# Performance work log

Hardware: AMD Instinct MI355X
Metric: run time of the kernel (lower is better)

The kernel has to match this reference:

```python
import jax, jax.numpy as jnp
import numpy as np

DIM = 512
HEADS = 8
HEAD_DIM = DIM // HEADS
SCALE = HEAD_DIM ** -0.5


def setup_inputs() -> dict:
    key = jax.random.key(0)
    ks = jax.random.split(key, 7)
    B, QN, N = 32, 128, 4096
    q = jax.random.normal(ks[0], (B, QN, DIM), dtype=jnp.float32)
    kv = jax.random.normal(ks[1], (B, N, DIM), dtype=jnp.float32)
    key_mask = jax.random.normal(ks[2], (B, QN, N), dtype=jnp.float32)
    Wq = jax.random.normal(ks[3], (DIM, DIM), dtype=jnp.float32) * 0.02
    Wkv = jax.random.normal(ks[4], (2 * DIM, DIM), dtype=jnp.float32) * 0.02
    Wproj = jax.random.normal(ks[5], (DIM, DIM), dtype=jnp.float32) * 0.02
    bproj = jax.random.normal(ks[6], (DIM,), dtype=jnp.float32) * 0.02
    return {"q": q, "kv": kv, "key_mask": key_mask,
            "Wq": Wq, "Wkv": Wkv, "Wproj": Wproj, "bproj": bproj}


def reference(q, kv, key_mask, Wq, Wkv, Wproj, bproj):
    B, QN, C = q.shape
    N = kv.shape[1]
    # q projection -> [B, QN, H, hd]
    qh = (q @ Wq.T).reshape(B, QN, HEADS, HEAD_DIM) * SCALE
    # kv projection -> split into k, v each [B, N, H, hd]
    kvp = kv @ Wkv.T  # [B, N, 2C]
    k = kvp[..., :C].reshape(B, N, HEADS, HEAD_DIM)
    v = kvp[..., C:].reshape(B, N, HEADS, HEAD_DIM)
    # scores [B, H, QN, N] + additive mask broadcast over heads
    attn = jnp.einsum('bqhd,bkhd->bhqk', qh, k) + key_mask[:, None]
    attn = jax.nn.softmax(attn, axis=-1)
    x = jnp.einsum('bhqk,bkhd->bqhd', attn, v).reshape(B, QN, C)
    return x @ Wproj.T + bproj
```

## Files before the change

### kernel.cpp

```cpp
#include <hip/hip_runtime.h>
#include <hip/hip_bf16.h>

typedef __attribute__((ext_vector_type(4))) float f32x4;
typedef __attribute__((ext_vector_type(8))) short bf16x8;

#define GAS __attribute__((address_space(1)))
#define LAS __attribute__((address_space(3)))

__device__ __forceinline__ unsigned int cvtpk(float lo, float hi) {
  unsigned int r;
  asm("v_cvt_pk_bf16_f32 %0, %1, %2" : "=v"(r) : "v"(lo), "v"(hi));
  return r;
}
__device__ __forceinline__ unsigned short f2bf(float f) { return (unsigned short)cvtpk(f, f); }
__device__ __forceinline__ f32x4 mfma16(bf16x8 a, bf16x8 b, f32x4 c) {
  return __builtin_amdgcn_mfma_f32_16x16x32_bf16(a, b, c, 0, 0, 0);
}
__device__ __forceinline__ void gl_lds16(const unsigned short* g, unsigned short* l) {
  __builtin_amdgcn_global_load_lds((const GAS unsigned short*)g, (LAS unsigned short*)l, 16, 0, 0);
}
__device__ __forceinline__ void memfence_sched() { asm volatile("" ::: "memory"); }

__global__ __launch_bounds__(256)
void cvt_f32_bf16(const float* __restrict__ in, unsigned short* __restrict__ out, int n8) {
  for (int i = blockIdx.x * blockDim.x + threadIdx.x; i < n8; i += gridDim.x * blockDim.x) {
    const float4 a = *reinterpret_cast<const float4*>(in + (size_t)i * 8);
    const float4 b = *reinterpret_cast<const float4*>(in + (size_t)i * 8 + 4);
    uint4 o;
    o.x = cvtpk(a.x, a.y); o.y = cvtpk(a.z, a.w);
    o.z = cvtpk(b.x, b.y); o.w = cvtpk(b.z, b.w);
    *reinterpret_cast<uint4*>(out + (size_t)i * 8) = o;
  }
}

template<int MODE, bool AF32, bool BF32>
__global__ __launch_bounds__(512, 2)
void gemm8(const void* __restrict__ Agv, const void* __restrict__ Bgv,
           void* __restrict__ Cg, const float* __restrict__ bias, int ntn, size_t ldc)
{
  constexpr bool MIXED = AF32 || BF32;
  constexpr int NA = MIXED ? 2 : 3;
  constexpr int NB = MIXED ? 2 : 3;
  __shared__ unsigned short sm[(NA + NB) * 8192];
  unsigned short* const smB = sm + NA * 8192;

  const int t = threadIdx.x, lane = t & 63, w = t >> 6;
  const int lo = lane & 15, hi = lane >> 4;
  const int wm = w >> 2, wn = w & 3;
  const int nwg = gridDim.x, bid = blockIdx.x;
  const int id = (bid & 7) * (nwg >> 3) + (bid >> 3);
  const int row0 = (id / ntn) * 256, col0 = (id % ntn) * 256;
  const int w16 = w * 16;

  const unsigned short* Ab = (const unsigned short*)Agv;
  const unsigned short* Bb = (const unsigned short*)Bgv;
  const float* Ff = AF32 ? (const float*)Agv : (const float*)Bgv;
  const int frow0 = AF32 ? row0 : col0;

  const int cxor_g = (lane >> 3) & 3;
  const size_t a_src_g = (size_t)(row0 + w16 + (lane >> 2)) * 512 + (((lane & 3) ^ cxor_g) << 3);
  const size_t b_src_g = (size_t)(col0 + w16 + (lane >> 2)) * 512 + (((lane & 3) ^ cxor_g) << 3);

  const int rs_r = t >> 2;
  const int rs_c = (t & 3) * 8;
  const int wch = ((t & 3) ^ ((t >> 3) & 3)) << 3;

  float4 stF[2][4];

  auto F_ISSUE = [&](int kt) {
    if constexpr (MIXED) {
      const int bk = kt & 1;
      const float* s0 = Ff + (size_t)(frow0 + rs_r) * 512 + kt * 32 + rs_c;
      const float* s1 = Ff + (size_t)(frow0 + 128 + rs_r) * 512 + kt * 32 + rs_c;
      stF[bk][0] = *(const float4*)s0; stF[bk][1] = *(const float4*)(s0 + 4);
      stF[bk][2] = *(const float4*)s1; stF[bk][3] = *(const float4*)(s1 + 4);
    }
  };
  auto F_WRITE = [&](int kt) {
    if constexpr (MIXED) {
      const int bk = kt & 1;
      unsigned short* fb = AF32 ? &sm[(kt % NA) * 8192] : &smB[(kt % NB) * 8192];
      uint4 o;
      o.x = cvtpk(stF[bk][0].x, stF[bk][0].y); o.y = cvtpk(stF[bk][0].z, stF[bk][0].w);
      o.z = cvtpk(stF[bk][1].x, stF[bk][1].y); o.w = cvtpk(stF[bk][1].z, stF[bk][1].w);
      *reinterpret_cast<uint4*>(&fb[rs_r * 32 + wch]) = o;
      o.x = cvtpk(stF[bk][2].x, stF[bk][2].y); o.y = cvtpk(stF[bk][2].z, stF[bk][2].w);
      o.z = cvtpk(stF[bk][3].x, stF[bk][3].y); o.w = cvtpk(stF[bk][3].z, stF[bk][3].w);
      *reinterpret_cast<uint4*>(&fb[(128 + rs_r) * 32 + wch]) = o;
    }
  };
  auto G_ISSUE = [&](int kt) {
    if constexpr (!AF32) {
      unsigned short* ab = &sm[(kt % NA) * 8192];
      gl_lds16(Ab + a_src_g + kt * 32, ab + w16 * 32);
      gl_lds16(Ab + a_src_g + (size_t)128 * 512 + kt * 32, ab + (128 + w16) * 32);
    }
    if constexpr (!BF32) {
      unsigned short* bb = &smB[(kt % NB) * 8192];
      gl_lds16(Bb + b_src_g + kt * 32, bb + w16 * 32);
      gl_lds16(Bb + b_src_g + (size_t)128 * 512 + kt * 32, bb + (128 + w16) * 32);
    }
  };

  f32x4 acc[8][4] = {};
  const int fxor = (hi ^ ((lo >> 1) & 3)) << 3;

  if constexpr (MIXED) {
    F_ISSUE(0);
    G_ISSUE(0);
    F_ISSUE(1);
    memfence_sched();
    asm volatile("s_waitcnt vmcnt(6)" ::: "memory");
    F_WRITE(0);
    asm volatile("s_waitcnt vmcnt(4)" ::: "memory");
  } else {
    G_ISSUE(0); G_ISSUE(1);
    memfence_sched();
    asm volatile("s_waitcnt vmcnt(4)" ::: "memory");
  }
  asm volatile("s_waitcnt lgkmcnt(0)" ::: "memory");
  __builtin_amdgcn_s_barrier();
  memfence_sched();

  #pragma unroll
  for (int kt = 0; kt < 16; ++kt) {
    const unsigned short* ab = &sm[(kt % NA) * 8192];
    const unsigned short* bb = &smB[(kt % NB) * 8192];
    bf16x8 bfr[4], af[4];
    #pragma unroll
    for (int nj = 0; nj < 4; ++nj)
      bfr[nj] = *reinterpret_cast<const bf16x8*>(&bb[(wn * 64 + nj * 16 + lo) * 32 + fxor]);
    #pragma unroll
    for (int mi = 0; mi < 4; ++mi)
      af[mi] = *reinterpret_cast<const bf16x8*>(&ab[(wm * 128 + mi * 16 + lo) * 32 + fxor]);

    if constexpr (MIXED) {
      if (kt <= 14) G_ISSUE(kt + 1);
      if (kt <= 13) F_ISSUE(kt + 2);
    } else {
      if (kt <= 13) G_ISSUE(kt + 2);
    }
    memfence_sched();

    __builtin_amdgcn_s_setprio(1);
    #pragma unroll
    for (int mi = 0; mi < 4; ++mi)
      #pragma unroll
      for (int nj = 0; nj < 4; ++nj)
        acc[mi][nj] = mfma16(af[mi], bfr[nj], acc[mi][nj]);
    __builtin_amdgcn_s_setprio(0);

    #pragma unroll
    for (int mi = 0; mi < 4; ++mi)
      af[mi] = *reinterpret_cast<const bf16x8*>(&ab[(wm * 128 + (mi + 4) * 16 + lo) * 32 + fxor]);

    if constexpr (MIXED) {
      if (kt <= 13)      { asm volatile("s_waitcnt vmcnt(6)" ::: "memory"); }
      else if (kt == 14) { asm volatile("s_waitcnt vmcnt(2)" ::: "memory"); }
      if (kt <= 14) F_WRITE(kt + 1);
    }

    __builtin_amdgcn_s_setprio(1);
    #pragma unroll
    for (int mi = 0; mi < 4; ++mi)
      #pragma unroll
      for (int nj = 0; nj < 4; ++nj)
        acc[mi + 4][nj] = mfma16(af[mi], bfr[nj], acc[mi + 4][nj]);
    __builtin_amdgcn_s_setprio(0);

    if (kt < 15) {
      if constexpr (MIXED) {
        if (kt <= 13)      { asm volatile("s_waitcnt vmcnt(4)" ::: "memory"); }
        else               { asm volatile("s_waitcnt vmcnt(0)" ::: "memory"); }
      } else {
        if (kt <= 13)      { asm volatile("s_waitcnt vmcnt(4)" ::: "memory"); }
        else               { asm volatile("s_waitcnt vmcnt(0)" ::: "memory"); }
      }
      asm volatile("s_waitcnt lgkmcnt(0)" ::: "memory");
      __builtin_amdgcn_s_barrier();
      memfence_sched();
    }
  }

  #pragma unroll
  for (int mi = 0; mi < 8; ++mi) {
    #pragma unroll
    for (int r = 0; r < 4; ++r) {
      const size_t gm = (size_t)row0 + wm * 128 + mi * 16 + hi * 4 + r;
      #pragma unroll
      for (int nj = 0; nj < 4; ++nj) {
        const int gn = col0 + wn * 64 + nj * 16 + lo;
        const float v = acc[mi][nj][r];
        if constexpr (MODE == 0)
          ((unsigned short*)Cg)[gm * ldc + gn] = f2bf(v * 0.125f);
        else if constexpr (MODE == 1)
          ((unsigned short*)Cg)[gm * ldc + gn] = f2bf(v);
        else
          ((float*)Cg)[gm * ldc + gn] = v + bias[gn];
      }
    }
  }
}

__global__ __launch_bounds__(256)
void attn_fwd(const unsigned short* __restrict__ qh,
              const unsigned short* __restrict__ kbuf,
              const unsigned short* __restrict__ vT,
              const float* __restrict__ mask,
              float* __restrict__ opart, float* __restrict__ ml)
{
  __shared__ unsigned short Ks[64 * 64];
  __shared__ unsigned short Vs[64 * 64];
  __shared__ unsigned short Ps[4][16 * 64];
  const int bid = blockIdx.x;
  const int xcd = bid & 7, g = bid >> 3;
  const int b = (g >> 6) * 8 + xcd;
  const int sub = g & 63;
  const int h = sub >> 3, qhalf = (sub >> 2) & 1, c = sub & 3;
  const int n0 = c * 1024;
  const int bh2 = (b * 8 + h) * 2 + qhalf;
  const int t = threadIdx.x, lane = t & 63, w = t >> 6;
  const int hi = lane >> 4, lo = lane & 15;
  const int q0 = qhalf * 64 + w * 16;

  bf16x8 aq[2];
  #pragma unroll
  for (int kk = 0; kk < 2; ++kk)
    aq[kk] = *reinterpret_cast<const bf16x8*>(
        qh + (size_t)(b * 128 + q0 + lo) * 512 + h * 64 + kk * 32 + hi * 8);

  float mrow[4], lrow[4];
  #pragma unroll
  for (int i = 0; i < 4; ++i) { mrow[i] = -1e30f; lrow[i] = 0.f; }
  f32x4 o[4] = {};

  const unsigned short* kp = kbuf + ((size_t)b * 4096 + n0) * 512 + h * 64;
  const unsigned short* vp = vT + (size_t)(h * 64) * 131072 + (size_t)b * 4096 + n0;
  const float* mp = mask + ((size_t)(b * 128 + q0)) * 4096 + n0;

  for (int nt = 0; nt < 16; ++nt) {
    {
      const int r = t >> 3, cc = t & 7;
      *reinterpret_cast<uint4*>(&Ks[r * 64 + ((cc ^ (r & 7)) << 3)]) =
          *reinterpret_cast<const uint4*>(kp + (size_t)(nt * 64 + r) * 512 + (cc << 3));
      *reinterpret_cast<uint4*>(&Ks[(r + 32) * 64 + ((cc ^ (r & 7)) << 3)]) =
          *reinterpret_cast<const uint4*>(kp + (size_t)(nt * 64 + r + 32) * 512 + (cc << 3));
      *reinterpret_cast<uint4*>(&Vs[r * 64 + ((cc ^ (r & 7)) << 3)]) =
          *reinterpret_cast<const uint4*>(vp + (size_t)r * 131072 + nt * 64 + (cc << 3));
      *reinterpret_cast<uint4*>(&Vs[(r + 32) * 64 + ((cc ^ (r & 7)) << 3)]) =
          *reinterpret_cast<const uint4*>(vp + (size_t)(r + 32) * 131072 + nt * 64 + (cc << 3));
    }
    __syncthreads();

    f32x4 s[4] = {};
    __builtin_amdgcn_s_setprio(1);
    #pragma unroll
    for (int ni = 0; ni < 4; ++ni) {
      #pragma unroll
      for (int kk = 0; kk < 2; ++kk) {
        const bf16x8 kf = *reinterpret_cast<const bf16x8*>(
            &Ks[(ni * 16 + lo) * 64 + ((kk * 32 + hi * 8) ^ ((lo & 7) << 3))]);
        s[ni] = mfma16(aq[kk], kf, s[ni]);
      }
    }
    __builtin_amdgcn_s_setprio(0);
    #pragma unroll
    for (int ni = 0; ni < 4; ++ni)
      #pragma unroll
      for (int r = 0; r < 4; ++r)
        s[ni][r] += mp[(size_t)(hi * 4 + r) * 4096 + nt * 64 + ni * 16 + lo];

    #pragma unroll
    for (int r = 0; r < 4; ++r) {
      float mx = fmaxf(fmaxf(s[0][r], s[1][r]), fmaxf(s[2][r], s[3][r]));
      #pragma unroll
      for (int off = 1; off < 16; off <<= 1)
        mx = fmaxf(mx, __shfl_xor(mx, off, 64));
      const float mnew = fmaxf(mrow[r], mx);
      const float corr = __expf(mrow[r] - mnew);
      mrow[r] = mnew;
      float ls = 0.f;
      #pragma unroll
      for (int ni = 0; ni < 4; ++ni) {
        const float p = __expf(s[ni][r] - mnew);
        s[ni][r] = p; ls += p;
      }
      #pragma unroll
      for (int off = 1; off < 16; off <<= 1)
        ls += __shfl_xor(ls, off, 64);
      lrow[r] = lrow[r] * corr + ls;
      #pragma unroll
      for (int di = 0; di < 4; ++di)
        o[di][r] *= corr;
    }

    #pragma unroll
    for (int ni = 0; ni < 4; ++ni)
      #pragma unroll
      for (int r = 0; r < 4; ++r) {
        const int rp = hi * 4 + r;
        Ps[w][rp * 64 + ((ni * 16 + lo) ^ ((rp & 7) << 3))] = f2bf(s[ni][r]);
      }

    __builtin_amdgcn_s_setprio(1);
    #pragma unroll
    for (int kk = 0; kk < 2; ++kk) {
      const bf16x8 pa = *reinterpret_cast<const bf16x8*>(
          &Ps[w][lo * 64 + ((kk * 32 + hi * 8) ^ ((lo & 7) << 3))]);
      #pragma unroll
      for (int di = 0; di < 4; ++di) {
        const bf16x8 vf = *reinterpret_cast<const bf16x8*>(
            &Vs[(di * 16 + lo) * 64 + ((kk * 32 + hi * 8) ^ ((lo & 7) << 3))]);
        o[di] = mfma16(pa, vf, o[di]);
      }
    }
    __builtin_amdgcn_s_setprio(0);
    __syncthreads();
  }

  const size_t pbase = ((size_t)bh2 * 4 + c) * 64;
  #pragma unroll
  for (int di = 0; di < 4; ++di)
    #pragma unroll
    for (int r = 0; r < 4; ++r)
      opart[(pbase + (w * 16 + hi * 4 + r)) * 64 + di * 16 + lo] = o[di][r];
  if (lo == 0) {
    #pragma unroll
    for (int r = 0; r < 4; ++r) {
      const int qq = w * 16 + hi * 4 + r;
      ml[(((size_t)bh2 * 4 + c) * 2 + 0) * 64 + qq] = mrow[r];
      ml[(((size_t)bh2 * 4 + c) * 2 + 1) * 64 + qq] = lrow[r];
    }
  }
}

__global__ __launch_bounds__(256)
void attn_combine(const float* __restrict__ opart, const float* __restrict__ ml,
                  unsigned short* __restrict__ xb)
{
  const int bh2 = blockIdx.x;
  const int b = bh2 >> 4, h = (bh2 >> 1) & 7, qhalf = bh2 & 1;
  const int t = threadIdx.x;
  const int q = t >> 2, dg = t & 3;

  float m[4], l[4];
  #pragma unroll
  for (int c = 0; c < 4; ++c) {
    m[c] = ml[(((size_t)bh2 * 4 + c) * 2 + 0) * 64 + q];
    l[c] = ml[(((size_t)bh2 * 4 + c) * 2 + 1) * 64 + q];
  }
  const float M = fmaxf(fmaxf(m[0], m[1]), fmaxf(m[2], m[3]));
  float sc[4], L = 0.f;
  #pragma unroll
  for (int c = 0; c < 4; ++c) { sc[c] = __expf(m[c] - M); L += sc[c] * l[c]; }
  const float inv = 1.f / L;

  float4 acc[4] = {};
  #pragma unroll
  for (int c = 0; c < 4; ++c) {
    const float* base = opart + (((size_t)bh2 * 4 + c) * 64 + q) * 64 + dg * 16;
    #pragma unroll
    for (int j = 0; j < 4; ++j) {
      const float4 v = *reinterpret_cast<const float4*>(base + j * 4);
      acc[j].x = fmaf(sc[c], v.x, acc[j].x);
      acc[j].y = fmaf(sc[c], v.y, acc[j].y);
      acc[j].z = fmaf(sc[c], v.z, acc[j].z);
      acc[j].w = fmaf(sc[c], v.w, acc[j].w);
    }
  }
  unsigned short* dst = xb + ((size_t)b * 128 + qhalf * 64 + q) * 512 + h * 64 + dg * 16;
  uint4 o1, o2;
  o1.x = cvtpk(acc[0].x * inv, acc[0].y * inv); o1.y = cvtpk(acc[0].z * inv, acc[0].w * inv);
  o1.z = cvtpk(acc[1].x * inv, acc[1].y * inv); o1.w = cvtpk(acc[1].z * inv, acc[1].w * inv);
  o2.x = cvtpk(acc[2].x * inv, acc[2].y * inv); o2.y = cvtpk(acc[2].z * inv, acc[2].w * inv);
  o2.z = cvtpk(acc[3].x * inv, acc[3].y * inv); o2.w = cvtpk(acc[3].z * inv, acc[3].w * inv);
  *reinterpret_cast<uint4*>(dst) = o1;
  *reinterpret_cast<uint4*>(dst + 8) = o2;
}

extern "C" void kernel_launch(void* const* d_in, const int* in_sizes, int n_in,
                              void* d_out, int out_size, void* d_ws, size_t ws_size,
                              hipStream_t stream) {
  const float* q     = (const float*)d_in[0];
  const float* kv    = (const float*)d_in[1];
  const float* mask  = (const float*)d_in[2];
  const float* Wq    = (const float*)d_in[3];
  const float* Wkv   = (const float*)d_in[4];
  const float* Wproj = (const float*)d_in[5];
  const float* bproj = (const float*)d_in[6];
  float* out = (float*)d_out;

  char* ws = (char*)d_ws;
  unsigned short* kbuf   = (unsigned short*)ws;
  unsigned short* vTb    = (unsigned short*)(ws + 134217728ULL);
  float*          opart  = (float*)(ws + 268435456ULL);
  float*          mlb    = (float*)(ws + 301989888ULL);
  unsigned short* qhb    = (unsigned short*)(ws + 303038464ULL);
  unsigned short* xb     = (unsigned short*)(ws + 307232768ULL);
  unsigned short* Wqb    = (unsigned short*)(ws + 311427072ULL);
  unsigned short* Wkvb   = (unsigned short*)(ws + 311951360ULL);
  unsigned short* Wprojb = (unsigned short*)(ws + 312999936ULL);

  cvt_f32_bf16<<<128, 256, 0, stream>>>(Wq, Wqb, 512 * 512 / 8);
  cvt_f32_bf16<<<256, 256, 0, stream>>>(Wkv, Wkvb, 1024 * 512 / 8);
  cvt_f32_bf16<<<128, 256, 0, stream>>>(Wproj, Wprojb, 512 * 512 / 8);

  gemm8<0, true, false><<<32, 512, 0, stream>>>(q, Wqb, qhb, nullptr, 2, 512);
  gemm8<1, true, false><<<1024, 512, 0, stream>>>(kv, Wkvb, kbuf, nullptr, 2, 512);
  gemm8<1, false, true><<<1024, 512, 0, stream>>>(Wkvb + 512 * 512, kv, vTb, nullptr, 512, 131072);
  attn_fwd<<<2048, 256, 0, stream>>>(qhb, kbuf, vTb, mask, opart, mlb);
  attn_combine<<<512, 256, 0, stream>>>(opart, mlb, xb);
  gemm8<2, false, false><<<32, 512, 0, stream>>>(xb, Wprojb, out, bproj, 2, 512);
}
```

Baseline: 448.9 us.

## Pre-convert activations to bf16 and use a pure-bf16 async-staged GEMM

Removes the fp32-input register staging path from the GEMM. q and kv are now converted to bf16 in separate passes, with kv done in two chunks that reuse the opart workspace. The GEMM now stages A and B separately through global_load_lds with a new LDS layout and a three-deep buffer ring, interleaving barriers between the half-tile MFMA phases. The extra conversion passes add an fp32 read and a bf16 write of kv. The GEMM loads become fully asynchronous, at the cost of more barriers per k-step.

```diff
diff --git a/kernel.cpp b/kernel.cpp
--- a/kernel.cpp
+++ b/kernel.cpp
@@ -33,115 +33,63 @@
   }
 }
 
-template<int MODE, bool AF32, bool BF32>
+template<int MODE>
 __global__ __launch_bounds__(512, 2)
-void gemm8(const void* __restrict__ Agv, const void* __restrict__ Bgv,
-           void* __restrict__ Cg, const float* __restrict__ bias, int ntn, size_t ldc)
+void gemm8p(const unsigned short* __restrict__ Ag, const unsigned short* __restrict__ Bg,
+            void* __restrict__ Cg, const float* __restrict__ bias, int ntn, size_t ldc)
 {
-  constexpr bool MIXED = AF32 || BF32;
-  constexpr int NA = MIXED ? 2 : 3;
-  constexpr int NB = MIXED ? 2 : 3;
-  __shared__ unsigned short sm[(NA + NB) * 8192];
-  unsigned short* const smB = sm + NA * 8192;
-
+  __shared__ unsigned short sm[49152];
   const int t = threadIdx.x, lane = t & 63, w = t >> 6;
   const int lo = lane & 15, hi = lane >> 4;
   const int wm = w >> 2, wn = w & 3;
   const int nwg = gridDim.x, bid = blockIdx.x;
   const int id = (bid & 7) * (nwg >> 3) + (bid >> 3);
   const int row0 = (id / ntn) * 256, col0 = (id % ntn) * 256;
-  const int w16 = w * 16;
-
-  const unsigned short* Ab = (const unsigned short*)Agv;
-  const unsigned short* Bb = (const unsigned short*)Bgv;
-  const float* Ff = AF32 ? (const float*)Agv : (const float*)Bgv;
-  const int frow0 = AF32 ? row0 : col0;
-
-  const int cxor_g = (lane >> 3) & 3;
-  const size_t a_src_g = (size_t)(row0 + w16 + (lane >> 2)) * 512 + (((lane & 3) ^ cxor_g) << 3);
-  const size_t b_src_g = (size_t)(col0 + w16 + (lane >> 2)) * 512 + (((lane & 3) ^ cxor_g) << 3);
-
-  const int rs_r = t >> 2;
-  const int rs_c = (t & 3) * 8;
-  const int wch = ((t & 3) ^ ((t >> 3) & 3)) << 3;
-
-  float4 stF[2][4];
-
-  auto F_ISSUE = [&](int kt) {
-    if constexpr (MIXED) {
-      const int bk = kt & 1;
-      const float* s0 = Ff + (size_t)(frow0 + rs_r) * 512 + kt * 32 + rs_c;
-      const float* s1 = Ff + (size_t)(frow0 + 128 + rs_r) * 512 + kt * 32 + rs_c;
-      stF[bk][0] = *(const float4*)s0; stF[bk][1] = *(const float4*)(s0 + 4);
-      stF[bk][2] = *(const float4*)s1; stF[bk][3] = *(const float4*)(s1 + 4);
-    }
+
+  const int gcol = ((t & 3) * 8) ^ (((t >> 5) & 1) << 4);
+  const int grow = t >> 2;
+  const unsigned short* aS = Ag + (size_t)(row0 + grow) * 512 + gcol;
+  const unsigned short* bS = Bg + (size_t)(col0 + grow) * 512 + gcol;
+  const int wds = w * 512;
+
+  auto STAGE_A = [&](int kt) {
+    const int bf = kt % 3;
+    gl_lds16(aS + kt * 32,         &sm[(bf * 2 + 0) * 4096 + wds]);
+    gl_lds16(aS + kt * 32 + 65536, &sm[(bf * 2 + 1) * 4096 + wds]);
   };
-  auto F_WRITE = [&](int kt) {
-    if constexpr (MIXED) {
-      const int bk = kt & 1;
-      unsigned short* fb = AF32 ? &sm[(kt % NA) * 8192] : &smB[(kt % NB) * 8192];
-      uint4 o;
-      o.x = cvtpk(stF[bk][0].x, stF[bk][0].y); o.y = cvtpk(stF[bk][0].z, stF[bk][0].w);
-      o.z = cvtpk(stF[bk][1].x, stF[bk][1].y); o.w = cvtpk(stF[bk][1].z, stF[bk][1].w);
-      *reinterpret_cast<uint4*>(&fb[rs_r * 32 + wch]) = o;
-      o.x = cvtpk(stF[bk][2].x, stF[bk][2].y); o.y = cvtpk(stF[bk][2].z, stF[bk][2].w);
-      o.z = cvtpk(stF[bk][3].x, stF[bk][3].y); o.w = cvtpk(stF[bk][3].z, stF[bk][3].w);
-      *reinterpret_cast<uint4*>(&fb[(128 + rs_r) * 32 + wch]) = o;
-    }
+  auto STAGE_B = [&](int kt) {
+    const int bf = kt % 3;
+    gl_lds16(bS + kt * 32,         &sm[24576 + (bf * 2 + 0) * 4096 + wds]);
+    gl_lds16(bS + kt * 32 + 65536, &sm[24576 + (bf * 2 + 1) * 4096 + wds]);
   };
-  auto G_ISSUE = [&](int kt) {
-    if constexpr (!AF32) {
-      unsigned short* ab = &sm[(kt % NA) * 8192];
-      gl_lds16(Ab + a_src_g + kt * 32, ab + w16 * 32);
-      gl_lds16(Ab + a_src_g + (size_t)128 * 512 + kt * 32, ab + (128 + w16) * 32);
-    }
-    if constexpr (!BF32) {
-      unsigned short* bb = &smB[(kt % NB) * 8192];
-      gl_lds16(Bb + b_src_g + kt * 32, bb + w16 * 32);
-      gl_lds16(Bb + b_src_g + (size_t)128 * 512 + kt * 32, bb + (128 + w16) * 32);
-    }
-  };
 
   f32x4 acc[8][4] = {};
-  const int fxor = (hi ^ ((lo >> 1) & 3)) << 3;
-
-  if constexpr (MIXED) {
-    F_ISSUE(0);
-    G_ISSUE(0);
-    F_ISSUE(1);
-    memfence_sched();
-    asm volatile("s_waitcnt vmcnt(6)" ::: "memory");
-    F_WRITE(0);
-    asm volatile("s_waitcnt vmcnt(4)" ::: "memory");
-  } else {
-    G_ISSUE(0); G_ISSUE(1);
-    memfence_sched();
-    asm volatile("s_waitcnt vmcnt(4)" ::: "memory");
-  }
-  asm volatile("s_waitcnt lgkmcnt(0)" ::: "memory");
+  const int fc = (hi * 8) ^ (((lo >> 3) & 1) << 4);
+  const int rbB = (wn & 1) * 64;
+
+  STAGE_A(0); STAGE_B(0); STAGE_A(1); STAGE_B(1);
+  memfence_sched();
+  asm volatile("s_waitcnt vmcnt(4)" ::: "memory");
   __builtin_amdgcn_s_barrier();
   memfence_sched();
 
   #pragma unroll
   for (int kt = 0; kt < 16; ++kt) {
-    const unsigned short* ab = &sm[(kt % NA) * 8192];
-    const unsigned short* bb = &smB[(kt % NB) * 8192];
+    const int bf = kt % 3;
+    const unsigned short* aB = &sm[(bf * 2 + wm) * 4096];
+    const unsigned short* bB = &sm[24576 + (bf * 2 + (wn >> 1)) * 4096];
+
     bf16x8 bfr[4], af[4];
     #pragma unroll
     for (int nj = 0; nj < 4; ++nj)
-      bfr[nj] = *reinterpret_cast<const bf16x8*>(&bb[(wn * 64 + nj * 16 + lo) * 32 + fxor]);
+      bfr[nj] = *reinterpret_cast<const bf16x8*>(&bB[(rbB + nj * 16 + lo) * 32 + fc]);
     #pragma unroll
     for (int mi = 0; mi < 4; ++mi)
-      af[mi] = *reinterpret_cast<const bf16x8*>(&ab[(wm * 128 + mi * 16 + lo) * 32 + fxor]);
-
-    if constexpr (MIXED) {
-      if (kt <= 14) G_ISSUE(kt + 1);
-      if (kt <= 13) F_ISSUE(kt + 2);
-    } else {
-      if (kt <= 13) G_ISSUE(kt + 2);
-    }
-    memfence_sched();
-
+      af[mi] = *reinterpret_cast<const bf16x8*>(&aB[(mi * 16 + lo) * 32 + fc]);
+    if (kt <= 13) STAGE_A(kt + 2);
+    memfence_sched();
+    __builtin_amdgcn_s_barrier();
+    memfence_sched();
     __builtin_amdgcn_s_setprio(1);
     #pragma unroll
     for (int mi = 0; mi < 4; ++mi)
@@ -149,17 +97,16 @@
       for (int nj = 0; nj < 4; ++nj)
         acc[mi][nj] = mfma16(af[mi], bfr[nj], acc[mi][nj]);
     __builtin_amdgcn_s_setprio(0);
+    __builtin_amdgcn_s_barrier();
+    memfence_sched();
 
     #pragma unroll
     for (int mi = 0; mi < 4; ++mi)
-      af[mi] = *reinterpret_cast<const bf16x8*>(&ab[(wm * 128 + (mi + 4) * 16 + lo) * 32 + fxor]);
-
-    if constexpr (MIXED) {
-      if (kt <= 13)      { asm volatile("s_waitcnt vmcnt(6)" ::: "memory"); }
-      else if (kt == 14) { asm volatile("s_waitcnt vmcnt(2)" ::: "memory"); }
-      if (kt <= 14) F_WRITE(kt + 1);
-    }
-
+      af[mi] = *reinterpret_cast<const bf16x8*>(&aB[((mi + 4) * 16 + lo) * 32 + fc]);
+    if (kt <= 13) STAGE_B(kt + 2);
+    memfence_sched();
+    __builtin_amdgcn_s_barrier();
+    memfence_sched();
     __builtin_amdgcn_s_setprio(1);
     #pragma unroll
     for (int mi = 0; mi < 4; ++mi)
@@ -167,19 +114,9 @@
       for (int nj = 0; nj < 4; ++nj)
         acc[mi + 4][nj] = mfma16(af[mi], bfr[nj], acc[mi + 4][nj]);
     __builtin_amdgcn_s_setprio(0);
-
-    if (kt < 15) {
-      if constexpr (MIXED) {
-        if (kt <= 13)      { asm volatile("s_waitcnt vmcnt(4)" ::: "memory"); }
-        else               { asm volatile("s_waitcnt vmcnt(0)" ::: "memory"); }
-      } else {
-        if (kt <= 13)      { asm volatile("s_waitcnt vmcnt(4)" ::: "memory"); }
-        else               { asm volatile("s_waitcnt vmcnt(0)" ::: "memory"); }
-      }
-      asm volatile("s_waitcnt lgkmcnt(0)" ::: "memory");
-      __builtin_amdgcn_s_barrier();
-      memfence_sched();
-    }
+    if (kt <= 13)      { asm volatile("s_waitcnt vmcnt(4)" ::: "memory"); }
+    else if (kt == 14) { asm volatile("s_waitcnt vmcnt(0)" ::: "memory"); }
+    if (kt < 15) { __builtin_amdgcn_s_barrier(); memfence_sched(); }
   }
 
   #pragma unroll
@@ -393,22 +330,33 @@
   char* ws = (char*)d_ws;
   unsigned short* kbuf   = (unsigned short*)ws;
   unsigned short* vTb    = (unsigned short*)(ws + 134217728ULL);
+  unsigned short* kvbfc  = (unsigned short*)(ws + 268435456ULL);
+  unsigned short* qbf    = kvbfc;
   float*          opart  = (float*)(ws + 268435456ULL);
   float*          mlb    = (float*)(ws + 301989888ULL);
-  unsigned short* qhb    = (unsigned short*)(ws + 303038464ULL);
-  unsigned short* xb     = (unsigned short*)(ws + 307232768ULL);
-  unsigned short* Wqb    = (unsigned short*)(ws + 311427072ULL);
-  unsigned short* Wkvb   = (unsigned short*)(ws + 311951360ULL);
-  unsigned short* Wprojb = (unsigned short*)(ws + 312999936ULL);
+  unsigned short* xb     = (unsigned short*)(ws + 303038464ULL);
+  unsigned short* qhb    = (unsigned short*)(ws + 335544320ULL);
+  unsigned short* Wqb    = (unsigned short*)(ws + 339738624ULL);
+  unsigned short* Wkvb   = (unsigned short*)(ws + 340262912ULL);
+  unsigned short* Wprojb = (unsigned short*)(ws + 341311488ULL);
 
   cvt_f32_bf16<<<128, 256, 0, stream>>>(Wq, Wqb, 512 * 512 / 8);
   cvt_f32_bf16<<<256, 256, 0, stream>>>(Wkv, Wkvb, 1024 * 512 / 8);
   cvt_f32_bf16<<<128, 256, 0, stream>>>(Wproj, Wprojb, 512 * 512 / 8);
 
-  gemm8<0, true, false><<<32, 512, 0, stream>>>(q, Wqb, qhb, nullptr, 2, 512);
-  gemm8<1, true, false><<<1024, 512, 0, stream>>>(kv, Wkvb, kbuf, nullptr, 2, 512);
-  gemm8<1, false, true><<<1024, 512, 0, stream>>>(Wkvb + 512 * 512, kv, vTb, nullptr, 512, 131072);
+  cvt_f32_bf16<<<256, 256, 0, stream>>>(q, qbf, 4096 * 512 / 8);
+  gemm8p<0><<<32, 512, 0, stream>>>(qbf, Wqb, qhb, nullptr, 2, 512);
+
+  for (int c = 0; c < 2; ++c) {
+    cvt_f32_bf16<<<2048, 256, 0, stream>>>(kv + (size_t)c * 65536 * 512, kvbfc,
+                                           65536 * 512 / 8);
+    gemm8p<1><<<512, 512, 0, stream>>>(kvbfc, Wkvb,
+                                       kbuf + (size_t)c * 65536 * 512, nullptr, 2, 512);
+    gemm8p<1><<<512, 512, 0, stream>>>(Wkvb + 512 * 512, kvbfc,
+                                       vTb + (size_t)c * 65536, nullptr, 256, 131072);
+  }
+
   attn_fwd<<<2048, 256, 0, stream>>>(qhb, kbuf, vTb, mask, opart, mlb);
   attn_combine<<<512, 256, 0, stream>>>(opart, mlb, xb);
-  gemm8<2, false, false><<<32, 512, 0, stream>>>(xb, Wprojb, out, bproj, 2, 512);
-}
+  gemm8p<2><<<32, 512, 0, stream>>>(xb, Wprojb, out, bproj, 2, 512);
+}
```

After: 439.7 us. 2.1% less time.

## Fuse K and V projection GEMMs into one kernel with LDS-staged transposed epilogue

Applied to the files above, without the earlier changes.

Replaces the separate K projection GEMM and the transposed V projection GEMM with a single GEMM over the full Wkv (N=1024), so the fp32 kv input is read and converted once instead of twice. The epilogue stages results through LDS: K tiles are written as row-major vectorized stores, and V tiles are transposed in LDS with an XOR swizzle and written as vT. This removes a whole pass over the large kv tensor. In exchange it adds LDS round trips and barriers in the epilogue, and the V stores become 8-byte writes into a strided transposed layout.

```diff
diff --git a/kernel.cpp b/kernel.cpp
--- a/kernel.cpp
+++ b/kernel.cpp
@@ -3,6 +3,7 @@
 
 typedef __attribute__((ext_vector_type(4))) float f32x4;
 typedef __attribute__((ext_vector_type(8))) short bf16x8;
+typedef __attribute__((ext_vector_type(4))) unsigned short ush4;
 
 #define GAS __attribute__((address_space(1)))
 #define LAS __attribute__((address_space(3)))
@@ -36,7 +37,8 @@
 template<int MODE, bool AF32, bool BF32>
 __global__ __launch_bounds__(512, 2)
 void gemm8(const void* __restrict__ Agv, const void* __restrict__ Bgv,
-           void* __restrict__ Cg, const float* __restrict__ bias, int ntn, size_t ldc)
+           void* __restrict__ Cg, void* __restrict__ Cg2,
+           const float* __restrict__ bias, int ntn, size_t ldc)
 {
   constexpr bool MIXED = AF32 || BF32;
   constexpr int NA = MIXED ? 2 : 3;
@@ -169,34 +171,75 @@
     __builtin_amdgcn_s_setprio(0);
 
     if (kt < 15) {
-      if constexpr (MIXED) {
-        if (kt <= 13)      { asm volatile("s_waitcnt vmcnt(4)" ::: "memory"); }
-        else               { asm volatile("s_waitcnt vmcnt(0)" ::: "memory"); }
-      } else {
-        if (kt <= 13)      { asm volatile("s_waitcnt vmcnt(4)" ::: "memory"); }
-        else               { asm volatile("s_waitcnt vmcnt(0)" ::: "memory"); }
-      }
+      if (kt <= 13)      { asm volatile("s_waitcnt vmcnt(4)" ::: "memory"); }
+      else               { asm volatile("s_waitcnt vmcnt(0)" ::: "memory"); }
       asm volatile("s_waitcnt lgkmcnt(0)" ::: "memory");
       __builtin_amdgcn_s_barrier();
       memfence_sched();
     }
   }
 
-  #pragma unroll
-  for (int mi = 0; mi < 8; ++mi) {
-    #pragma unroll
-    for (int r = 0; r < 4; ++r) {
-      const size_t gm = (size_t)row0 + wm * 128 + mi * 16 + hi * 4 + r;
-      #pragma unroll
-      for (int nj = 0; nj < 4; ++nj) {
-        const int gn = col0 + wn * 64 + nj * 16 + lo;
-        const float v = acc[mi][nj][r];
-        if constexpr (MODE == 0)
-          ((unsigned short*)Cg)[gm * ldc + gn] = f2bf(v * 0.125f);
-        else if constexpr (MODE == 1)
-          ((unsigned short*)Cg)[gm * ldc + gn] = f2bf(v);
-        else
-          ((float*)Cg)[gm * ldc + gn] = v + bias[gn];
+  if constexpr (MODE == 3) {
+    __syncthreads();
+    unsigned short* Tb = &sm[w * 4096];
+    if (col0 < 512) {
+      #pragma unroll
+      for (int p = 0; p < 2; ++p) {
+        #pragma unroll
+        for (int q = 0; q < 4; ++q)
+          #pragma unroll
+          for (int nj = 0; nj < 4; ++nj)
+            #pragma unroll
+            for (int r = 0; r < 4; ++r)
+              Tb[(q * 16 + hi * 4 + r) * 64 + nj * 16 + lo] = f2bf(acc[p * 4 + q][nj][r]);
+        #pragma unroll
+        for (int it = 0; it < 8; ++it) {
+          const int rr = it * 8 + (lane >> 3);
+          const bf16x8 v = *reinterpret_cast<const bf16x8*>(&Tb[rr * 64 + (lane & 7) * 8]);
+          const size_t gm = (size_t)row0 + wm * 128 + p * 64 + rr;
+          *reinterpret_cast<bf16x8*>((unsigned short*)Cg + gm * 512 + col0 + wn * 64 +
+                                     (lane & 7) * 8) = v;
+        }
+      }
+    } else {
+      #pragma unroll
+      for (int p = 0; p < 2; ++p) {
+        #pragma unroll
+        for (int q = 0; q < 4; ++q)
+          #pragma unroll
+          for (int nj = 0; nj < 4; ++nj)
+            #pragma unroll
+            for (int r = 0; r < 4; ++r) {
+              const int gn_l = nj * 16 + lo;
+              const int gm_l = (q * 16 + hi * 4 + r) ^ ((gn_l & 15) * 4);
+              Tb[gn_l * 64 + gm_l] = f2bf(acc[p * 4 + q][nj][r]);
+            }
+        #pragma unroll
+        for (int it = 0; it < 16; ++it) {
+          const int gn_l = it * 4 + (lane >> 4);
+          const int g4 = ((lane & 15) * 4) ^ ((gn_l & 15) * 4);
+          const ush4 v = *reinterpret_cast<const ush4*>(&Tb[gn_l * 64 + g4]);
+          const size_t vrow = (size_t)(col0 - 512) + wn * 64 + gn_l;
+          const size_t vcol = (size_t)row0 + wm * 128 + p * 64 + (lane & 15) * 4;
+          *reinterpret_cast<ush4*>((unsigned short*)Cg2 + vrow * 131072 + vcol) = v;
+        }
+      }
+    }
+  } else {
+    #pragma unroll
+    for (int mi = 0; mi < 8; ++mi) {
+      #pragma unroll
+      for (int r = 0; r < 4; ++r) {
+        const size_t gm = (size_t)row0 + wm * 128 + mi * 16 + hi * 4 + r;
+        #pragma unroll
+        for (int nj = 0; nj < 4; ++nj) {
+          const int gn = col0 + wn * 64 + nj * 16 + lo;
+          const float v = acc[mi][nj][r];
+          if constexpr (MODE == 0)
+            ((unsigned short*)Cg)[gm * ldc + gn] = f2bf(v * 0.125f);
+          else
+            ((float*)Cg)[gm * ldc + gn] = v + bias[gn];
+        }
       }
     }
   }
@@ -405,10 +448,9 @@
   cvt_f32_bf16<<<256, 256, 0, stream>>>(Wkv, Wkvb, 1024 * 512 / 8);
   cvt_f32_bf16<<<128, 256, 0, stream>>>(Wproj, Wprojb, 512 * 512 / 8);
 
-  gemm8<0, true, false><<<32, 512, 0, stream>>>(q, Wqb, qhb, nullptr, 2, 512);
-  gemm8<1, true, false><<<1024, 512, 0, stream>>>(kv, Wkvb, kbuf, nullptr, 2, 512);
-  gemm8<1, false, true><<<1024, 512, 0, stream>>>(Wkvb + 512 * 512, kv, vTb, nullptr, 512, 131072);
+  gemm8<0, true, false><<<32, 512, 0, stream>>>(q, Wqb, qhb, nullptr, nullptr, 2, 512);
+  gemm8<3, true, false><<<2048, 512, 0, stream>>>(kv, Wkvb, kbuf, vTb, nullptr, 4, 512);
   attn_fwd<<<2048, 256, 0, stream>>>(qhb, kbuf, vTb, mask, opart, mlb);
   attn_combine<<<512, 256, 0, stream>>>(opart, mlb, xb);
-  gemm8<2, false, false><<<32, 512, 0, stream>>>(xb, Wprojb, out, bproj, 2, 512);
-}
+  gemm8<2, false, false><<<32, 512, 0, stream>>>(xb, Wprojb, out, nullptr, bproj, 2, 512);
+}
```

After: 432.0 us. -3.8%, faster.
